# Optimization experiments

Hardware: AMD Instinct MI355X
Metric: run time of the kernel (lower is better)

The kernel has to match this reference:

```python
import jax, jax.numpy as jnp
import numpy as np

N_NODES = 50000
N_EDGES = 600000
D_FEAT = 128


def setup_inputs() -> dict:
    key = jax.random.key(0)
    k_h, k_src, k_dst, k_dt, k_norm = jax.random.split(key, 5)
    h = jax.random.normal(k_h, (N_NODES, D_FEAT), dtype=jnp.float32)
    src = jax.random.randint(k_src, (N_EDGES,), 0, N_NODES, dtype=jnp.int32)
    dst = jax.random.randint(k_dst, (N_EDGES,), 0, N_NODES, dtype=jnp.int32)
    # dt: non-negative time deltas (scaled up a bit so the decay matters)
    dt = jax.random.uniform(k_dt, (N_EDGES,), dtype=jnp.float32) * 10.0
    # norm: symmetric-normalization-like positive edge weights
    norm = jax.random.uniform(k_norm, (N_EDGES,), dtype=jnp.float32)
    decay_lam = jnp.full((1,), 0.1, dtype=jnp.float32)  # nn.Parameter(0.1)
    return {"h": h, "src": src, "dst": dst, "dt": dt, "norm": norm, "decay_lam": decay_lam}


def reference(h, src, dst, dt, norm, decay_lam):
    # lam = relu(decay_lam) + 1e-4  (scalar)
    lam = jax.nn.relu(decay_lam[0]) + 1e-4
    # per-edge temporal weight: norm * exp(-lam * dt)   [E]
    w = norm * jnp.exp(-lam * dt)
    # u_mul_e: gather source features, scale by edge weight  [E, D]
    m = h[src] * w[:, None]
    # sum-reduce messages at destination nodes  [N, D]
    h_new = jax.ops.segment_sum(m, dst, num_segments=h.shape[0])
    return h_new
```

## Files before the change

### kernel.cpp

```cpp
#include <hip/hip_runtime.h>
#include <hip/hip_bf16.h>

#define D_FEAT 128
#define BIN_SHIFT 7
#define NODES_PER_BIN 128
#define BCAP 4096
#define EPB 2048
#define T1 512
#define HCAP 64
#define CSR_L_CAP 4608
#define OVF_CAP 4096

typedef float f2v __attribute__((ext_vector_type(2)));

__device__ __forceinline__ unsigned bf16_rne(float f) {
    unsigned u = __float_as_uint(f);
    return (u + 0x7fffu + ((u >> 16) & 1u)) >> 16;
}

__global__ void __launch_bounds__(T1)
conv_bin_kernel(const float* __restrict__ h,
                const int* __restrict__ src, const int* __restrict__ dst,
                const float* __restrict__ dt, const float* __restrict__ norm,
                const float* __restrict__ decay_lam,
                unsigned* __restrict__ hb,
                int* __restrict__ bin_cursor, unsigned long long* __restrict__ binned,
                int* __restrict__ ovf_cnt, int* __restrict__ ovf_d,
                int* __restrict__ ovf_s, float* __restrict__ ovf_w,
                int E, int HN4, int convBlocks, int NB) {
    __shared__ unsigned hist[T1];
    __shared__ unsigned cur[T1];
    __shared__ unsigned gbase[T1];

    int t = threadIdx.x;
    if (blockIdx.x < convBlocks) {
        int i = blockIdx.x * T1 + t;
        if (i < HN4) {
            float4 v = ((const float4*)h)[i];
            ((uint2*)hb)[i] = make_uint2(bf16_rne(v.x) | (bf16_rne(v.y) << 16),
                                         bf16_rne(v.z) | (bf16_rne(v.w) << 16));
        }
        return;
    }

    int e0 = (blockIdx.x - convBlocks) * EPB;

    hist[t] = 0; cur[t] = 0;
    __syncthreads();

    float lam = fmaxf(decay_lam[0], 0.0f) + 1e-4f;

    unsigned long long ent[EPB / T1];
    int bn[EPB / T1];
    #pragma unroll
    for (int k = 0; k < EPB / T1; ++k) {
        int e = e0 + k * T1 + t;
        bn[k] = -1;
        if (e < E) {
            int s = src[e], d = dst[e];
            float w = norm[e] * expf(-lam * dt[e]);
            int b = d >> BIN_SHIFT;
            int l = d & (NODES_PER_BIN - 1);
            ent[k] = ((unsigned long long)l << 32) | (((unsigned)s << 16) | bf16_rne(w));
            bn[k] = b;
            atomicAdd(&hist[b], 1u);
        }
    }
    __syncthreads();

    if (t < NB && hist[t] > 0)
        gbase[t] = (unsigned)atomicAdd(&bin_cursor[t], (int)hist[t]);
    __syncthreads();

    #pragma unroll
    for (int k = 0; k < EPB / T1; ++k) {
        if (bn[k] >= 0) {
            int b = bn[k];
            unsigned gp = gbase[b] + atomicAdd(&cur[b], 1u);
            if (gp < BCAP) {
                binned[(size_t)b * BCAP + gp] = ent[k];
            } else {
                int o = atomicAdd(ovf_cnt, 1);
                if (o < OVF_CAP) {
                    int l = (int)(ent[k] >> 32);
                    ovf_d[o] = (b << BIN_SHIFT) | l;
                    ovf_s[o] = (int)((ent[k] >> 16) & 0xFFFFu);
                    ovf_w[o] = __uint_as_float(((unsigned)ent[k] & 0xFFFFu) << 16);
                }
            }
        }
    }
}

__global__ void __launch_bounds__(T1)
sort_gather_kernel(const unsigned long long* __restrict__ binned,
                   const int* __restrict__ bin_cursor,
                   const unsigned* __restrict__ hb,
                   const int* __restrict__ ovf_cnt, const int* __restrict__ ovf_d,
                   const int* __restrict__ ovf_s, const float* __restrict__ ovf_w,
                   float* __restrict__ out, int N) {
    __shared__ unsigned hist[HCAP];
    __shared__ unsigned padoff[HCAP];
    __shared__ unsigned cur[HCAP];
    __shared__ unsigned csr_l[CSR_L_CAP];

    int b    = blockIdx.x >> 1;
    int half = blockIdx.x & 1;
    int t = threadIdx.x;
    int cnt = min(bin_cursor[b], BCAP);

    if (t < HCAP) { hist[t] = 0; cur[t] = 0; }
    for (int i = t; i < CSR_L_CAP; i += T1) csr_l[i] = 0;
    __syncthreads();

    unsigned long long ent[BCAP / T1];
    size_t base_in = (size_t)b * BCAP;
    #pragma unroll
    for (int k = 0; k < BCAP / T1; ++k) {
        int idx = k * T1 + t;
        ent[k] = ~0ull;
        if (idx < cnt) {
            unsigned long long e = binned[base_in + idx];
            int l = (int)(e >> 32);
            if ((l >> 6) == half) {
                ent[k] = e;
                atomicAdd(&hist[l & (HCAP - 1)], 1u);
            }
        }
    }
    __syncthreads();

    unsigned pc = 0, val = 0;
    if (t < HCAP) { pc = (hist[t] + 7u) & ~7u; val = pc; }
    #pragma unroll
    for (int off = 1; off < HCAP; off <<= 1) {
        unsigned u = __shfl_up(val, off, 64);
        if ((t & 63) >= off) val += u;
    }
    if (t < HCAP) padoff[t] = val - pc;
    __syncthreads();

    #pragma unroll
    for (int k = 0; k < BCAP / T1; ++k) {
        if (ent[k] != ~0ull) {
            int l = (int)(ent[k] >> 32) & (HCAP - 1);
            unsigned p = padoff[l] + atomicAdd(&cur[l], 1u);
            csr_l[p] = (unsigned)ent[k];
        }
    }
    __syncthreads();

    int wid = t >> 6;
    int lane = t & 63;
    int base_node = (b << BIN_SHIFT) + half * HCAP;
    int nodes = min(HCAP, N - base_node);
    bool ovf_bin = bin_cursor[b] > BCAP;

    for (int l = wid; l < nodes; l += 8) {
        unsigned base = padoff[l];
        unsigned mr = (hist[l] + 7u) & ~7u;
        float accx = 0.0f, accy = 0.0f;
        for (unsigned j = 0; j < mr; j += 8) {
            unsigned u0 = csr_l[base + j + 0];
            unsigned u1 = csr_l[base + j + 1];
            unsigned u2 = csr_l[base + j + 2];
            unsigned u3 = csr_l[base + j + 3];
            unsigned u4 = csr_l[base + j + 4];
            unsigned u5 = csr_l[base + j + 5];
            unsigned u6 = csr_l[base + j + 6];
            unsigned u7 = csr_l[base + j + 7];
            unsigned v0 = hb[(size_t)(u0 >> 16) * 64 + lane];
            unsigned v1 = hb[(size_t)(u1 >> 16) * 64 + lane];
            unsigned v2 = hb[(size_t)(u2 >> 16) * 64 + lane];
            unsigned v3 = hb[(size_t)(u3 >> 16) * 64 + lane];
            unsigned v4 = hb[(size_t)(u4 >> 16) * 64 + lane];
            unsigned v5 = hb[(size_t)(u5 >> 16) * 64 + lane];
            unsigned v6 = hb[(size_t)(u6 >> 16) * 64 + lane];
            unsigned v7 = hb[(size_t)(u7 >> 16) * 64 + lane];
            #define ACC(u, v)                                             \
            {   float wf = __uint_as_float((u) << 16);                    \
                float vx = __uint_as_float((v) << 16);                    \
                float vy = __uint_as_float((v) & 0xffff0000u);            \
                accx += vx * wf; accy += vy * wf; }
            ACC(u0, v0) ACC(u1, v1) ACC(u2, v2) ACC(u3, v3)
            ACC(u4, v4) ACC(u5, v5) ACC(u6, v6) ACC(u7, v7)
            #undef ACC
        }
        int node = base_node + l;
        if (ovf_bin) {
            int oc = min(*ovf_cnt, OVF_CAP);
            for (int o = 0; o < oc; ++o) {
                if (ovf_d[o] == node) {
                    float we = ovf_w[o];
                    unsigned v = hb[(size_t)ovf_s[o] * 64 + lane];
                    accx += __uint_as_float(v << 16) * we;
                    accy += __uint_as_float(v & 0xffff0000u) * we;
                }
            }
        }
        f2v r;
        r.x = accx; r.y = accy;
        __builtin_nontemporal_store(r, (f2v*)(out + (size_t)node * D_FEAT) + lane);
    }
}


__global__ void degree_kernel(const int* __restrict__ dst, int* __restrict__ deg, int E) {
    int e = blockIdx.x * blockDim.x + threadIdx.x;
    if (e >= E) return;
    atomicAdd(&deg[dst[e]], 1);
}

__global__ void scan_blocks(const int* __restrict__ deg, int* __restrict__ offs,
                            int* __restrict__ blockSums, int N) {
    __shared__ int tmp[256];
    int tid = threadIdx.x;
    int gid = blockIdx.x * 256 + tid;
    int v = (gid < N) ? deg[gid] : 0;
    tmp[tid] = v;
    __syncthreads();
    for (int off = 1; off < 256; off <<= 1) {
        int t = (tid >= off) ? tmp[tid - off] : 0;
        __syncthreads();
        tmp[tid] += t;
        __syncthreads();
    }
    if (gid < N) offs[gid] = tmp[tid] - v;
    if (tid == 255) blockSums[blockIdx.x] = tmp[255];
}

__global__ void scan_sums(int* __restrict__ blockSums, int* __restrict__ blockOffs, int nb) {
    __shared__ int tmp[256];
    int tid = threadIdx.x;
    int v = (tid < nb) ? blockSums[tid] : 0;
    tmp[tid] = v;
    __syncthreads();
    for (int off = 1; off < 256; off <<= 1) {
        int t = (tid >= off) ? tmp[tid - off] : 0;
        __syncthreads();
        tmp[tid] += t;
        __syncthreads();
    }
    if (tid < nb) blockOffs[tid] = tmp[tid] - v;
}

__global__ void scan_fixup(int* __restrict__ offs, const int* __restrict__ blockOffs,
                           int* __restrict__ cursor, int N) {
    int gid = blockIdx.x * 256 + threadIdx.x;
    if (gid >= N) return;
    int o = offs[gid] + blockOffs[blockIdx.x];
    offs[gid] = o;
    cursor[gid] = o;
}

__global__ void bucket_kernel(const int* __restrict__ src, const int* __restrict__ dst,
                              const float* __restrict__ dt, const float* __restrict__ norm,
                              const float* __restrict__ decay_lam,
                              int* __restrict__ cursor, float2* __restrict__ pairs, int E) {
    int e = blockIdx.x * blockDim.x + threadIdx.x;
    if (e >= E) return;
    float lam = fmaxf(decay_lam[0], 0.0f) + 1e-4f;
    float w = norm[e] * expf(-lam * dt[e]);
    int d = dst[e];
    int pos = atomicAdd(&cursor[d], 1);
    float2 p;
    p.x = __int_as_float(src[e]);
    p.y = w;
    pairs[pos] = p;
}

__global__ void __launch_bounds__(256)
gather_kernel(const float* __restrict__ h,
              const int* __restrict__ offs, const int* __restrict__ deg,
              const float2* __restrict__ pairs, float* __restrict__ out, int N) {
    int node = blockIdx.x * 4 + (threadIdx.x >> 6);
    if (node >= N) return;
    int lane = threadIdx.x & 63;
    int start = offs[node];
    int end = start + deg[node];
    float accx = 0.0f, accy = 0.0f;
    for (int j = start; j < end; ++j) {
        float2 p = pairs[j];
        int s = __float_as_int(p.x);
        float we = p.y;
        float2 v = ((const float2*)(h + (size_t)s * D_FEAT))[lane];
        accx += v.x * we;
        accy += v.y * we;
    }
    float2 r; r.x = accx; r.y = accy;
    ((float2*)(out + (size_t)node * D_FEAT))[lane] = r;
}

extern "C" void kernel_launch(void* const* d_in, const int* in_sizes, int n_in,
                              void* d_out, int out_size, void* d_ws, size_t ws_size,
                              hipStream_t stream) {
    const float* h         = (const float*)d_in[0];
    const int*   src       = (const int*)d_in[1];
    const int*   dst       = (const int*)d_in[2];
    const float* dt        = (const float*)d_in[3];
    const float* norm      = (const float*)d_in[4];
    const float* decay_lam = (const float*)d_in[5];
    float* out = (float*)d_out;

    const int E  = in_sizes[1];
    const int HN = in_sizes[0];
    const int N  = out_size / D_FEAT;
    const int NB = (N + NODES_PER_BIN - 1) >> BIN_SHIFT;

    auto align64 = [](size_t x) { return (x + 63) & ~(size_t)63; };
    size_t sz_binc = align64((size_t)NB * 4);
    size_t sz_ovfc = 64;
    size_t sz_ovf  = align64((size_t)OVF_CAP * 4);
    size_t sz_binn = align64((size_t)NB * BCAP * 8);
    size_t sz_hb   = align64((size_t)HN * 2);
    size_t need = sz_binc + sz_ovfc + 3 * sz_ovf + sz_binn + sz_hb;

    if (ws_size >= need && N <= 65536 && (HN & 3) == 0 && NB <= T1) {
        char* ws = (char*)d_ws;
        int* bin_cursor = (int*)ws;                 ws += sz_binc;
        int* ovf_cnt    = (int*)ws;                 ws += sz_ovfc;
        int* ovf_d      = (int*)ws;                 ws += sz_ovf;
        int* ovf_s      = (int*)ws;                 ws += sz_ovf;
        float* ovf_w    = (float*)ws;               ws += sz_ovf;
        unsigned long long* binned = (unsigned long long*)ws;  ws += sz_binn;
        unsigned* hb    = (unsigned*)ws;

        hipMemsetAsync(bin_cursor, 0, sz_binc + sz_ovfc, stream);

        const int HN4 = HN / 4;
        const int convBlocks = (HN4 + T1 - 1) / T1;
        const int binBlocks  = (E + EPB - 1) / EPB;
        conv_bin_kernel<<<convBlocks + binBlocks, T1, 0, stream>>>(
            h, src, dst, dt, norm, decay_lam, hb, bin_cursor, binned,
            ovf_cnt, ovf_d, ovf_s, ovf_w, E, HN4, convBlocks, NB);

        sort_gather_kernel<<<NB * 2, T1, 0, stream>>>(
            binned, bin_cursor, hb, ovf_cnt, ovf_d, ovf_s, ovf_w, out, N);
    } else {
        const int nb = (N + 255) / 256;
        char* ws = (char*)d_ws;
        int*    dega      = (int*)ws;     ws += (size_t)N * 4;
        int*    offsa     = (int*)ws;     ws += (size_t)N * 4;
        int*    cursor    = (int*)ws;     ws += (size_t)N * 4;
        int*    blockSums = (int*)ws;     ws += 256 * 4;
        int*    blockOffs = (int*)ws;     ws += 256 * 4;
        float2* pairs     = (float2*)ws;

        hipMemsetAsync(dega, 0, (size_t)N * 4, stream);
        degree_kernel<<<(E + 255) / 256, 256, 0, stream>>>(dst, dega, E);
        scan_blocks<<<nb, 256, 0, stream>>>(dega, offsa, blockSums, N);
        scan_sums<<<1, 256, 0, stream>>>(blockSums, blockOffs, nb);
        scan_fixup<<<nb, 256, 0, stream>>>(offsa, blockOffs, cursor, N);
        bucket_kernel<<<(E + 255) / 256, 256, 0, stream>>>(
            src, dst, dt, norm, decay_lam, cursor, pairs, E);
        gather_kernel<<<(N + 3) / 4, 256, 0, stream>>>(h, offsa, dega, pairs, out, N);
    }
}
```

Before: 128.1 us.

## Fuse memset, binning and gather into one cooperative persistent kernel

Replaces the memset plus two kernel launches with a single cooperative kernel that zeroes counters, converts features and bins edges, then sorts and gathers per bin, using grid-wide syncs between phases. This removes launch overhead and inter-kernel gaps. In exchange, the grid is capped by occupancy, so fewer concurrent blocks loop over virtual blocks, and the larger shared-memory footprint may lower occupancy. If the cooperative launch fails it falls back to the old path.

Result: slower. 214.5 us (+67.5%).

```diff
diff --git a/kernel.cpp b/kernel.cpp
--- a/kernel.cpp
+++ b/kernel.cpp
@@ -1,5 +1,8 @@
 #include <hip/hip_runtime.h>
+#include <hip/hip_cooperative_groups.h>
 #include <hip/hip_bf16.h>
+
+namespace cg = cooperative_groups;
 
 #define D_FEAT 128
 #define BIN_SHIFT 7
@@ -17,6 +20,199 @@
     unsigned u = __float_as_uint(f);
     return (u + 0x7fffu + ((u >> 16) & 1u)) >> 16;
 }
+
+__global__ void __launch_bounds__(T1)
+fused_kernel(const float* __restrict__ h,
+             const int* __restrict__ src, const int* __restrict__ dst,
+             const float* __restrict__ dt, const float* __restrict__ norm,
+             const float* __restrict__ decay_lam,
+             unsigned* __restrict__ hb,
+             int* __restrict__ bin_cursor, unsigned long long* __restrict__ binned,
+             int* __restrict__ ovf_cnt, int* __restrict__ ovf_d,
+             int* __restrict__ ovf_s, float* __restrict__ ovf_w,
+             float* __restrict__ out,
+             int E, int HN4, int convBlocks, int binBlocks, int NB, int N) {
+    cg::grid_group grid = cg::this_grid();
+
+    __shared__ unsigned hist1[T1];
+    __shared__ unsigned cur1[T1];
+    __shared__ unsigned gbase1[T1];
+    __shared__ unsigned hist2[HCAP];
+    __shared__ unsigned padoff2[HCAP];
+    __shared__ unsigned cur2[HCAP];
+    __shared__ unsigned csr_l[CSR_L_CAP];
+
+    int t = threadIdx.x;
+
+    for (int i = blockIdx.x * T1 + t; i < NB; i += gridDim.x * T1)
+        bin_cursor[i] = 0;
+    if (blockIdx.x == 0 && t == 0) *ovf_cnt = 0;
+    grid.sync();
+
+    float lam = fmaxf(decay_lam[0], 0.0f) + 1e-4f;
+    int p1end = convBlocks + binBlocks;
+    for (int vb = blockIdx.x; vb < p1end; vb += gridDim.x) {
+        if (vb < convBlocks) {
+            int i = vb * T1 + t;
+            if (i < HN4) {
+                float4 v = ((const float4*)h)[i];
+                ((uint2*)hb)[i] = make_uint2(bf16_rne(v.x) | (bf16_rne(v.y) << 16),
+                                             bf16_rne(v.z) | (bf16_rne(v.w) << 16));
+            }
+        } else {
+            int e0 = (vb - convBlocks) * EPB;
+            hist1[t] = 0; cur1[t] = 0;
+            __syncthreads();
+
+            unsigned long long ent[EPB / T1];
+            int bn[EPB / T1];
+            #pragma unroll
+            for (int k = 0; k < EPB / T1; ++k) {
+                int e = e0 + k * T1 + t;
+                bn[k] = -1;
+                if (e < E) {
+                    int s = src[e], d = dst[e];
+                    float w = norm[e] * expf(-lam * dt[e]);
+                    int b = d >> BIN_SHIFT;
+                    int l = d & (NODES_PER_BIN - 1);
+                    ent[k] = ((unsigned long long)l << 32) |
+                             (((unsigned)s << 16) | bf16_rne(w));
+                    bn[k] = b;
+                    atomicAdd(&hist1[b], 1u);
+                }
+            }
+            __syncthreads();
+
+            if (t < NB && hist1[t] > 0)
+                gbase1[t] = (unsigned)atomicAdd(&bin_cursor[t], (int)hist1[t]);
+            __syncthreads();
+
+            #pragma unroll
+            for (int k = 0; k < EPB / T1; ++k) {
+                if (bn[k] >= 0) {
+                    int b = bn[k];
+                    unsigned gp = gbase1[b] + atomicAdd(&cur1[b], 1u);
+                    if (gp < BCAP) {
+                        binned[(size_t)b * BCAP + gp] = ent[k];
+                    } else {
+                        int o = atomicAdd(ovf_cnt, 1);
+                        if (o < OVF_CAP) {
+                            int l = (int)(ent[k] >> 32);
+                            ovf_d[o] = (b << BIN_SHIFT) | l;
+                            ovf_s[o] = (int)((ent[k] >> 16) & 0xFFFFu);
+                            ovf_w[o] = __uint_as_float(((unsigned)ent[k] & 0xFFFFu) << 16);
+                        }
+                    }
+                }
+            }
+            __syncthreads();
+        }
+    }
+    grid.sync();
+
+    int p2end = NB * 2;
+    for (int vb = blockIdx.x; vb < p2end; vb += gridDim.x) {
+        int b    = vb >> 1;
+        int half = vb & 1;
+        int cnt = min(bin_cursor[b], BCAP);
+
+        if (t < HCAP) { hist2[t] = 0; cur2[t] = 0; }
+        for (int i = t; i < CSR_L_CAP; i += T1) csr_l[i] = 0;
+        __syncthreads();
+
+        unsigned long long ent[BCAP / T1];
+        size_t base_in = (size_t)b * BCAP;
+        #pragma unroll
+        for (int k = 0; k < BCAP / T1; ++k) {
+            int idx = k * T1 + t;
+            ent[k] = ~0ull;
+            if (idx < cnt) {
+                unsigned long long e = binned[base_in + idx];
+                int l = (int)(e >> 32);
+                if ((l >> 6) == half) {
+                    ent[k] = e;
+                    atomicAdd(&hist2[l & (HCAP - 1)], 1u);
+                }
+            }
+        }
+        __syncthreads();
+
+        unsigned pc = 0, val = 0;
+        if (t < HCAP) { pc = (hist2[t] + 7u) & ~7u; val = pc; }
+        #pragma unroll
+        for (int off = 1; off < HCAP; off <<= 1) {
+            unsigned u = __shfl_up(val, off, 64);
+            if ((t & 63) >= off) val += u;
+        }
+        if (t < HCAP) padoff2[t] = val - pc;
+        __syncthreads();
+
+        #pragma unroll
+        for (int k = 0; k < BCAP / T1; ++k) {
+            if (ent[k] != ~0ull) {
+                int l = (int)(ent[k] >> 32) & (HCAP - 1);
+                unsigned p = padoff2[l] + atomicAdd(&cur2[l], 1u);
+                csr_l[p] = (unsigned)ent[k];
+            }
+        }
+        __syncthreads();
+
+        int wid = t >> 6;
+        int lane = t & 63;
+        int base_node = (b << BIN_SHIFT) + half * HCAP;
+        int nodes = min(HCAP, N - base_node);
+        bool ovf_bin = bin_cursor[b] > BCAP;
+
+        for (int l = wid; l < nodes; l += 8) {
+            unsigned base = padoff2[l];
+            unsigned mr = (hist2[l] + 7u) & ~7u;
+            float accx = 0.0f, accy = 0.0f;
+            for (unsigned j = 0; j < mr; j += 8) {
+                unsigned u0 = csr_l[base + j + 0];
+                unsigned u1 = csr_l[base + j + 1];
+                unsigned u2 = csr_l[base + j + 2];
+                unsigned u3 = csr_l[base + j + 3];
+                unsigned u4 = csr_l[base + j + 4];
+                unsigned u5 = csr_l[base + j + 5];
+                unsigned u6 = csr_l[base + j + 6];
+                unsigned u7 = csr_l[base + j + 7];
+                unsigned v0 = hb[(size_t)(u0 >> 16) * 64 + lane];
+                unsigned v1 = hb[(size_t)(u1 >> 16) * 64 + lane];
+                unsigned v2 = hb[(size_t)(u2 >> 16) * 64 + lane];
+                unsigned v3 = hb[(size_t)(u3 >> 16) * 64 + lane];
+                unsigned v4 = hb[(size_t)(u4 >> 16) * 64 + lane];
+                unsigned v5 = hb[(size_t)(u5 >> 16) * 64 + lane];
+                unsigned v6 = hb[(size_t)(u6 >> 16) * 64 + lane];
+                unsigned v7 = hb[(size_t)(u7 >> 16) * 64 + lane];
+                #define ACC(u, v)                                             \
+                {   float wf = __uint_as_float((u) << 16);                    \
+                    float vx = __uint_as_float((v) << 16);                    \
+                    float vy = __uint_as_float((v) & 0xffff0000u);            \
+                    accx += vx * wf; accy += vy * wf; }
+                ACC(u0, v0) ACC(u1, v1) ACC(u2, v2) ACC(u3, v3)
+                ACC(u4, v4) ACC(u5, v5) ACC(u6, v6) ACC(u7, v7)
+                #undef ACC
+            }
+            int node = base_node + l;
+            if (ovf_bin) {
+                int oc = min(*ovf_cnt, OVF_CAP);
+                for (int o = 0; o < oc; ++o) {
+                    if (ovf_d[o] == node) {
+                        float we = ovf_w[o];
+                        unsigned v = hb[(size_t)ovf_s[o] * 64 + lane];
+                        accx += __uint_as_float(v << 16) * we;
+                        accy += __uint_as_float(v & 0xffff0000u) * we;
+                    }
+                }
+            }
+            f2v r;
+            r.x = accx; r.y = accy;
+            __builtin_nontemporal_store(r, (f2v*)(out + (size_t)node * D_FEAT) + lane);
+        }
+        __syncthreads();
+    }
+}
+
 
 __global__ void __launch_bounds__(T1)
 conv_bin_kernel(const float* __restrict__ h,
@@ -325,15 +521,47 @@
         unsigned long long* binned = (unsigned long long*)ws;  ws += sz_binn;
         unsigned* hb    = (unsigned*)ws;
 
+        const int HN4 = HN / 4;
+        int convBlocks = (HN4 + T1 - 1) / T1;
+        int binBlocks  = (E + EPB - 1) / EPB;
+
+        static int coopGrid = -2;
+        if (coopGrid == -2) {
+            int dev = 0;
+            hipGetDevice(&dev);
+            hipDeviceProp_t props{};
+            if (hipGetDeviceProperties(&props, dev) == hipSuccess &&
+                props.cooperativeLaunch) {
+                int perCU = 0;
+                if (hipOccupancyMaxActiveBlocksPerMultiprocessor(
+                        &perCU, reinterpret_cast<const void*>(fused_kernel),
+                        T1, 0) == hipSuccess && perCU > 0) {
+                    long g = (long)perCU * props.multiProcessorCount;
+                    if (g > 1024) g = 1024;
+                    coopGrid = (int)g;
+                } else coopGrid = -1;
+            } else coopGrid = -1;
+            (void)hipGetLastError();
+        }
+
+        if (coopGrid > 0) {
+            int E_ = E, HN4_ = HN4, cb_ = convBlocks, bb_ = binBlocks,
+                NB_ = NB, N_ = N;
+            void* args[] = { &h, &src, &dst, &dt, &norm, &decay_lam,
+                             &hb, &bin_cursor, &binned,
+                             &ovf_cnt, &ovf_d, &ovf_s, &ovf_w, &out,
+                             &E_, &HN4_, &cb_, &bb_, &NB_, &N_ };
+            hipError_t le = hipLaunchCooperativeKernel(
+                reinterpret_cast<const void*>(fused_kernel),
+                dim3(coopGrid), dim3(T1), args, 0, stream);
+            if (le == hipSuccess) return;
+            (void)hipGetLastError();
+        }
+
         hipMemsetAsync(bin_cursor, 0, sz_binc + sz_ovfc, stream);
-
-        const int HN4 = HN / 4;
-        const int convBlocks = (HN4 + T1 - 1) / T1;
-        const int binBlocks  = (E + EPB - 1) / EPB;
         conv_bin_kernel<<<convBlocks + binBlocks, T1, 0, stream>>>(
             h, src, dst, dt, norm, decay_lam, hb, bin_cursor, binned,
             ovf_cnt, ovf_d, ovf_s, ovf_w, E, HN4, convBlocks, NB);
-
         sort_gather_kernel<<<NB * 2, T1, 0, stream>>>(
             binned, bin_cursor, hb, ovf_cnt, ovf_d, ovf_s, ovf_w, out, N);
     } else {
```
